# Optimization experiments

Hardware: AMD Instinct MI355X
Metric: run time of the kernel (lower is better)

## Reference

```python
import jax, jax.numpy as jnp
import numpy as np

LEAKY_SLOPE = 0.2  # tf.nn.leaky_relu default alpha


def setup_inputs() -> dict:
    key = jax.random.key(0)
    k1, k2, k3 = jax.random.split(key, 3)
    B, T, K, D = 64, 2048, 256, 256  # batch, timesteps, n_nodes, out_dim
    inputs = jax.random.normal(k1, (B, T, K), dtype=jnp.float32)
    W = jax.random.normal(k2, (K, D), dtype=jnp.float32) * (1.0 / np.sqrt(K))
    a = jax.random.normal(k3, (2 * D, 1), dtype=jnp.float32) * (1.0 / np.sqrt(2 * D))
    return {"inputs": inputs, "W": W, "a": a}


def reference(inputs, W, a):
    # inputs: (B, T, K); W: (K, D); a: (2D, 1)
    B, T, K = inputs.shape
    D = W.shape[1]
    H = jnp.matmul(inputs, W)  # (B, T, D)
    # Original: H_concat[b,t,k] = concat([H[b,t], H[b,t]]) for every k (both
    # repeats are of the same H), so H_concat @ a == H @ (a_i + a_j), constant in k.
    a_i = a[:D, 0]
    a_j = a[D:, 0]
    e = jax.nn.leaky_relu(H @ (a_i + a_j), negative_slope=LEAKY_SLOPE)  # (B, T)
    e = jnp.broadcast_to(e[:, :, None], (B, T, K))  # (B, T, K) -- constant along K
    alpha = jax.nn.softmax(e, axis=2)  # exactly uniform 1/K
    # sum_k alpha[b,t,k] * H[b,t,d]  (H_repeat_i[b,t,k,:] == H[b,t,:])
    H_gat = jnp.einsum('btk,btd->btd', alpha, H)  # (B, T, D)
    return H_gat
```

## Files before the change

kernel.cpp:

```cpp
#include <hip/hip_runtime.h>
#include <cstdint>


static constexpr int MTOT = 64 * 2048;
static constexpr int KDIM = 256;
static constexpr int NDIM = 256;

typedef __bf16 bf16x8 __attribute__((ext_vector_type(8)));
typedef float f32x4 __attribute__((ext_vector_type(4)));

__device__ __forceinline__ uint32_t f2bf_pk(float a, float b) {
    uint32_t ua = __float_as_uint(a);
    uint32_t ub = __float_as_uint(b);
    ua = ua + 0x7fffu + ((ua >> 16) & 1u);
    ub = ub + 0x7fffu + ((ub >> 16) & 1u);
    return (ua >> 16) | (ub & 0xffff0000u);
}

__global__ void wt_transpose(const float* __restrict__ W, unsigned short* __restrict__ Wt) {
    int n = blockIdx.x;
    int k = threadIdx.x;
    float v = W[k * NDIM + n];
    uint32_t u = __float_as_uint(v);
    u = u + 0x7fffu + ((u >> 16) & 1u);
    Wt[n * KDIM + k] = (unsigned short)(u >> 16);
}

__global__ __launch_bounds__(1024, 1)
void gat_gemm(const float* __restrict__ A, const unsigned short* __restrict__ Wt,
              float* __restrict__ C) {
    __shared__ alignas(16) unsigned short Bs[128 * 256];
    __shared__ alignas(16) unsigned short As[2][256 * 64];

    const int tid  = threadIdx.x;
    const int lane = tid & 63;
    const int wave = tid >> 6;
    const int l15  = lane & 15;
    const int quad = lane >> 4;
    const int wm   = wave & 7;
    const int wn   = wave >> 3;

    const int b     = blockIdx.x;
    const int nhalf = (b >> 3) & 1;
    const int mt    = (b & 7) | ((b >> 4) << 3);
    const int bm    = mt * 256;
    const int bn    = nhalf * 128;

    const int arow = tid >> 3;
    const int aseg = tid & 7;

    const float* ap0 = A + (size_t)(bm + arow) * KDIM + aseg * 8;
    float4 a0 = *(const float4*)(ap0);
    float4 a1 = *(const float4*)(ap0 + 4);
    float4 a2 = *(const float4*)(ap0 + 128 * KDIM);
    float4 a3 = *(const float4*)(ap0 + 128 * KDIM + 4);

#pragma unroll
    for (int c = 0; c < 4; ++c) {
        int idx = c * 1024 + tid;
        int n   = idx >> 5;
        int kc  = idx & 31;
        uint4 v = *(const uint4*)(Wt + (size_t)(bn + n) * KDIM + kc * 8);
        *(uint4*)((char*)Bs + n * 512 + ((kc * 16) ^ ((n & 7) << 4))) = v;
    }

    {
        uint4 w;
        w.x = f2bf_pk(a0.x, a0.y); w.y = f2bf_pk(a0.z, a0.w);
        w.z = f2bf_pk(a1.x, a1.y); w.w = f2bf_pk(a1.z, a1.w);
        *(uint4*)((char*)&As[0][0] + arow * 128 + ((aseg * 16) ^ ((arow & 7) << 4))) = w;
        int r2 = arow + 128;
        w.x = f2bf_pk(a2.x, a2.y); w.y = f2bf_pk(a2.z, a2.w);
        w.z = f2bf_pk(a3.x, a3.y); w.w = f2bf_pk(a3.z, a3.w);
        *(uint4*)((char*)&As[0][0] + r2 * 128 + ((aseg * 16) ^ ((r2 & 7) << 4))) = w;
    }
    __syncthreads();

    f32x4 acc[2][4];
#pragma unroll
    for (int i = 0; i < 2; ++i)
#pragma unroll
        for (int j = 0; j < 4; ++j)
            acc[i][j] = (f32x4)0.0f;

#pragma unroll
    for (int kt = 0; kt < 4; ++kt) {
        float4 n0, n1, n2, n3;
        if (kt < 3) {
            const float* ap = A + (size_t)(bm + arow) * KDIM + (kt + 1) * 64 + aseg * 8;
            n0 = *(const float4*)(ap);
            n1 = *(const float4*)(ap + 4);
            n2 = *(const float4*)(ap + 128 * KDIM);
            n3 = *(const float4*)(ap + 128 * KDIM + 4);
        }

        const char* asb = (const char*)&As[kt & 1][0];
#pragma unroll
        for (int ks = 0; ks < 2; ++ks) {
            bf16x8 af[2];
#pragma unroll
            for (int i = 0; i < 2; ++i) {
                const int row = wm * 32 + i * 16 + l15;
                af[i] = *(const bf16x8*)(asb + row * 128 +
                          ((ks * 64 + quad * 16) ^ ((row & 7) << 4)));
            }
#pragma unroll
            for (int j = 0; j < 4; ++j) {
                const int n = wn * 64 + j * 16 + l15;
                bf16x8 bf = *(const bf16x8*)((const char*)Bs + n * 512 +
                              ((kt * 128 + ks * 64 + quad * 16) ^ ((n & 7) << 4)));
#pragma unroll
                for (int i = 0; i < 2; ++i)
                    acc[i][j] = __builtin_amdgcn_mfma_f32_16x16x32_bf16(af[i], bf, acc[i][j], 0, 0, 0);
            }
        }

        if (kt < 3) {
            char* dst = (char*)&As[(kt + 1) & 1][0];
            uint4 w;
            w.x = f2bf_pk(n0.x, n0.y); w.y = f2bf_pk(n0.z, n0.w);
            w.z = f2bf_pk(n1.x, n1.y); w.w = f2bf_pk(n1.z, n1.w);
            *(uint4*)(dst + arow * 128 + ((aseg * 16) ^ ((arow & 7) << 4))) = w;
            int r2 = arow + 128;
            w.x = f2bf_pk(n2.x, n2.y); w.y = f2bf_pk(n2.z, n2.w);
            w.z = f2bf_pk(n3.x, n3.y); w.w = f2bf_pk(n3.z, n3.w);
            *(uint4*)(dst + r2 * 128 + ((aseg * 16) ^ ((r2 & 7) << 4))) = w;
            __syncthreads();
        }
    }

#pragma unroll
    for (int i = 0; i < 2; ++i) {
#pragma unroll
        for (int r = 0; r < 4; ++r) {
            const size_t row = (size_t)(bm + wm * 32 + i * 16 + quad * 4 + r);
            float* cp = C + row * NDIM + bn + wn * 64 + l15;
#pragma unroll
            for (int j = 0; j < 4; ++j)
                cp[j * 16] = acc[i][j][r];
        }
    }
}

extern "C" void kernel_launch(void* const* d_in, const int* in_sizes, int n_in,
                              void* d_out, int out_size, void* d_ws, size_t ws_size,
                              hipStream_t stream) {
    (void)in_sizes; (void)n_in; (void)out_size; (void)ws_size;
    const float* inputs = (const float*)d_in[0];
    const float* W      = (const float*)d_in[1];
    unsigned short* Wt = (unsigned short*)d_ws;
    float* out = (float*)d_out;

    hipLaunchKernelGGL(wt_transpose, dim3(NDIM), dim3(KDIM), 0, stream, W, Wt);
    hipLaunchKernelGGL(gat_gemm, dim3((MTOT / 256) * 2), dim3(1024), 0, stream, inputs, Wt, out);
}
```

Baseline: 238.8 us.

## Prefetch two A k-tiles ahead with lighter barriers in bf16 GEMM

Restructures the A-operand pipeline so global loads for k-tiles are issued two steps ahead into rotating register sets (R0/R1), with the first two tiles and the W tile loaded before any shared-memory writes. The A load mapping changes to 16 threads per row, each loading one float4 across four row groups. `__syncthreads` is replaced by an explicit lgkmcnt wait plus s_barrier. The aim is to hide global-load latency on the memory-bound input stream, at the cost of more live registers.

Measured after the change: 237.0 us. About the same (-0.8%).

```diff
diff --git a/kernel.cpp b/kernel.cpp
--- a/kernel.cpp
+++ b/kernel.cpp
@@ -46,35 +46,9 @@
     const int bm    = mt * 256;
     const int bn    = nhalf * 128;
 
-    const int arow = tid >> 3;
-    const int aseg = tid & 7;
-
-    const float* ap0 = A + (size_t)(bm + arow) * KDIM + aseg * 8;
-    float4 a0 = *(const float4*)(ap0);
-    float4 a1 = *(const float4*)(ap0 + 4);
-    float4 a2 = *(const float4*)(ap0 + 128 * KDIM);
-    float4 a3 = *(const float4*)(ap0 + 128 * KDIM + 4);
-
-#pragma unroll
-    for (int c = 0; c < 4; ++c) {
-        int idx = c * 1024 + tid;
-        int n   = idx >> 5;
-        int kc  = idx & 31;
-        uint4 v = *(const uint4*)(Wt + (size_t)(bn + n) * KDIM + kc * 8);
-        *(uint4*)((char*)Bs + n * 512 + ((kc * 16) ^ ((n & 7) << 4))) = v;
-    }
-
-    {
-        uint4 w;
-        w.x = f2bf_pk(a0.x, a0.y); w.y = f2bf_pk(a0.z, a0.w);
-        w.z = f2bf_pk(a1.x, a1.y); w.w = f2bf_pk(a1.z, a1.w);
-        *(uint4*)((char*)&As[0][0] + arow * 128 + ((aseg * 16) ^ ((arow & 7) << 4))) = w;
-        int r2 = arow + 128;
-        w.x = f2bf_pk(a2.x, a2.y); w.y = f2bf_pk(a2.z, a2.w);
-        w.z = f2bf_pk(a3.x, a3.y); w.w = f2bf_pk(a3.z, a3.w);
-        *(uint4*)((char*)&As[0][0] + r2 * 128 + ((aseg * 16) ^ ((r2 & 7) << 4))) = w;
-    }
-    __syncthreads();
+    const int arow = tid >> 4;
+    const int acol = (tid & 15) * 4;
+    const int as8  = (tid & 15) * 8;
 
     f32x4 acc[2][4];
 #pragma unroll
@@ -83,18 +57,23 @@
         for (int j = 0; j < 4; ++j)
             acc[i][j] = (f32x4)0.0f;
 
+    auto issueA = [&](int kt, float4 (&R)[4]) {
 #pragma unroll
-    for (int kt = 0; kt < 4; ++kt) {
-        float4 n0, n1, n2, n3;
-        if (kt < 3) {
-            const float* ap = A + (size_t)(bm + arow) * KDIM + (kt + 1) * 64 + aseg * 8;
-            n0 = *(const float4*)(ap);
-            n1 = *(const float4*)(ap + 4);
-            n2 = *(const float4*)(ap + 128 * KDIM);
-            n3 = *(const float4*)(ap + 128 * KDIM + 4);
+        for (int i = 0; i < 4; ++i)
+            R[i] = *(const float4*)(A + (size_t)(bm + i * 64 + arow) * KDIM + kt * 64 + acol);
+    };
+    auto writeA = [&](unsigned short* dst, float4 (&R)[4]) {
+#pragma unroll
+        for (int i = 0; i < 4; ++i) {
+            const int r = i * 64 + arow;
+            uint2 w;
+            w.x = f2bf_pk(R[i].x, R[i].y);
+            w.y = f2bf_pk(R[i].z, R[i].w);
+            *(uint2*)((char*)dst + r * 128 + (as8 ^ ((r & 7) << 4))) = w;
         }
-
-        const char* asb = (const char*)&As[kt & 1][0];
+    };
+    auto compute = [&](const unsigned short* asrc, int kt) {
+        const char* asb = (const char*)asrc;
 #pragma unroll
         for (int ks = 0; ks < 2; ++ks) {
             bf16x8 af[2];
@@ -114,18 +93,40 @@
                     acc[i][j] = __builtin_amdgcn_mfma_f32_16x16x32_bf16(af[i], bf, acc[i][j], 0, 0, 0);
             }
         }
+    };
+    auto wavebar = [&]() {
+        asm volatile("s_waitcnt lgkmcnt(0)" ::: "memory");
+        __builtin_amdgcn_s_barrier();
+        asm volatile("" ::: "memory");
+    };
 
+    uint4 bv[4];
+#pragma unroll
+    for (int c = 0; c < 4; ++c) {
+        const int idx = c * 1024 + tid;
+        bv[c] = *(const uint4*)(Wt + (size_t)(bn + (idx >> 5)) * KDIM + (idx & 31) * 8);
+    }
+    float4 R0[4], R1[4];
+    issueA(0, R0);
+    issueA(1, R1);
+#pragma unroll
+    for (int c = 0; c < 4; ++c) {
+        const int idx = c * 1024 + tid;
+        const int n = idx >> 5, kc = idx & 31;
+        *(uint4*)((char*)Bs + n * 512 + ((kc * 16) ^ ((n & 7) << 4))) = bv[c];
+    }
+    writeA(&As[0][0], R0);
+    wavebar();
+
+#pragma unroll
+    for (int kt = 0; kt < 4; ++kt) {
+        if (kt < 2) {
+            if ((kt & 1) == 0) issueA(kt + 2, R0); else issueA(kt + 2, R1);
+        }
+        compute(&As[kt & 1][0], kt);
         if (kt < 3) {
-            char* dst = (char*)&As[(kt + 1) & 1][0];
-            uint4 w;
-            w.x = f2bf_pk(n0.x, n0.y); w.y = f2bf_pk(n0.z, n0.w);
-            w.z = f2bf_pk(n1.x, n1.y); w.w = f2bf_pk(n1.z, n1.w);
-            *(uint4*)(dst + arow * 128 + ((aseg * 16) ^ ((arow & 7) << 4))) = w;
-            int r2 = arow + 128;
-            w.x = f2bf_pk(n2.x, n2.y); w.y = f2bf_pk(n2.z, n2.w);
-            w.z = f2bf_pk(n3.x, n3.y); w.w = f2bf_pk(n3.z, n3.w);
-            *(uint4*)(dst + r2 * 128 + ((aseg * 16) ^ ((r2 & 7) << 4))) = w;
-            __syncthreads();
+            if ((kt & 1) == 0) writeA(&As[1][0], R1); else writeA(&As[0][0], R0);
+            wavebar();
         }
     }
 
```
